# Kernel optimization log

Measured on AMD Instinct MI355X. Metric: run time of the kernel, lower is better.

## Reference

```python
import jax, jax.numpy as jnp
import numpy as np

B, S, V = 256, 512, 50000
E, PD, PS = 256, 32, 121
FN, TAG = 230, 53
FEAT = E + 2 * PD  # 320
NEG = -1e30


def setup_inputs() -> dict:
    key = jax.random.key(0)
    ks = jax.random.split(key, 12)
    sentence = jax.random.randint(ks[0], (B, S), 0, V)
    # relative-position ids; 60 marks the entity token, keep background < 60
    pos1 = jax.random.randint(ks[1], (B, S), 0, 60)
    pos2 = jax.random.randint(ks[2], (B, S), 0, 60)
    e1 = jax.random.randint(ks[3], (B,), 1, S // 3)            # entity1 in first third
    e2 = jax.random.randint(ks[4], (B,), S // 3 + 1, 2 * S // 3)  # entity2 in second third
    rows = jnp.arange(B)
    pos1 = pos1.at[rows, e1].set(60)
    pos2 = pos2.at[rows, e2].set(60)
    word_emb = 0.02 * jax.random.normal(ks[5], (V, E), dtype=jnp.float32)
    pos1_emb = 0.02 * jax.random.normal(ks[6], (PS, PD), dtype=jnp.float32)
    pos2_emb = 0.02 * jax.random.normal(ks[7], (PS, PD), dtype=jnp.float32)
    rel_emb = 0.02 * jax.random.normal(ks[8], (TAG, FN), dtype=jnp.float32)
    conv_w = 0.05 * jax.random.normal(ks[9], (3, FEAT, FN), dtype=jnp.float32)  # HIO
    conv_b = jnp.zeros((FN,), dtype=jnp.float32)
    att_weight = jax.random.normal(ks[10], (B, 1, FN), dtype=jnp.float32)
    relation_bias = jax.random.normal(ks[11], (B, TAG, 1), dtype=jnp.float32)
    return {"sentence": sentence, "pos1": pos1, "pos2": pos2,
            "word_emb": word_emb, "pos1_emb": pos1_emb, "pos2_emb": pos2_emb,
            "rel_emb": rel_emb, "conv_w": conv_w, "conv_b": conv_b,
            "att_weight": att_weight, "relation_bias": relation_bias}


def reference(sentence, pos1, pos2, word_emb, pos1_emb, pos2_emb,
              rel_emb, conv_w, conv_b, att_weight, relation_bias):
    # embedding concat: [B, S, FEAT]
    embeds = jnp.concatenate(
        [word_emb[sentence], pos1_emb[pos1], pos2_emb[pos2]], axis=2)
    # Conv2d(1, FN, (3, FEAT), padding=(1, 0)) == 1D conv over seq, SAME-ish pad 1
    cnn = jax.lax.conv_general_dilated(
        embeds, conv_w, window_strides=(1,), padding=[(1, 1)],
        dimension_numbers=("NHC", "HIO", "NHC"))  # [B, S, FN]
    cnn = jax.nn.relu(cnn + conv_b)

    # vectorized entity segment boundaries (replaces the Python batch loop)
    idx = jnp.arange(S)
    mk1 = pos1 == 60
    mk2 = pos2 == 60
    p1min = jnp.min(jnp.where(mk1, idx, S), axis=1)
    p1max = jnp.max(jnp.where(mk1, idx, -1), axis=1)
    p2min = jnp.min(jnp.where(mk2, idx, S), axis=1)
    p2max = jnp.max(jnp.where(mk2, idx, -1), axis=1)
    first = p1min < p2min
    m1 = jnp.where(first, p1min, p2min)
    m2 = jnp.where(first, p1max, p2max)
    m3 = jnp.where(first, p2min, p1min)
    m4 = jnp.where(first, p2max, p1max)

    t = idx[None, :]  # [1, S]
    mask_a = t < jnp.maximum(m1, 1)[:, None]
    mask_b = (t >= m2[:, None]) & (t < jnp.maximum(m3, m2 + 1)[:, None])
    mask_c = t >= m4[:, None]

    def seg_max(mask):
        return jnp.max(jnp.where(mask[:, :, None], cnn, NEG), axis=1)  # [B, FN]

    pcnn = jnp.stack([seg_max(mask_a), seg_max(mask_b), seg_max(mask_c)], axis=2)  # [B, FN, 3]

    # attention over the 3 pooled segments
    M = jnp.tanh(pcnn)
    scores = jnp.einsum("bof,bft->bot", att_weight, M)      # [B, 1, 3]
    a = jax.nn.softmax(scores, axis=2)
    att = jnp.einsum("bft,bot->bfo", pcnn, a)               # [B, FN, 1]
    att_out = jnp.tanh(att)

    wei = jnp.einsum("tf,bfo->bto", rel_emb, att_out)       # [B, TAG, 1]
    res = jax.nn.softmax(wei + relation_bias, axis=1)
    return res.reshape(B, -1)
```

## Files before the change

### kernel.cpp

```cpp
#include <hip/hip_runtime.h>
#include <math.h>

constexpr int B    = 256;
constexpr int S    = 512;
constexpr int E    = 256;
constexpr int PD   = 32;
constexpr int FN   = 230;
constexpr int FNP  = 256;
constexpr int TAG  = 53;
constexpr int BM   = 128;
constexpr int NG   = 10;

typedef short  bf16x8 __attribute__((ext_vector_type(8)));
typedef float  f32x4  __attribute__((ext_vector_type(4)));

__device__ __forceinline__ unsigned f2bf(float x) {
    union { float f; unsigned u; } v; v.f = x;
    unsigned r = v.u + 0x7FFF + ((v.u >> 16) & 1);
    return r >> 16;
}
__device__ __forceinline__ unsigned pack2(float a, float b) {
    return f2bf(a) | (f2bf(b) << 16);
}

__device__ __forceinline__ void gl_lds16(const void* g, void* l) {
    __builtin_amdgcn_global_load_lds(
        (const __attribute__((address_space(1))) unsigned int*)g,
        (__attribute__((address_space(3))) unsigned int*)l, 16, 0, 0);
}

constexpr size_t WS_SEGB  = 0;
constexpr size_t WS_PCNN  = 4096;
constexpr size_t WS_WT3   = 790528;
constexpr size_t WS_ZERO  = 1282048;
constexpr size_t WS_WEMB  = 1282304;
constexpr size_t WS_P1H   = 26882304;
constexpr size_t WS_P2H   = 26890048;

__global__ __launch_bounds__(256) void prep_kernel(
    const float* __restrict__ conv_w, const int* __restrict__ pos1,
    const int* __restrict__ pos2,
    const float* __restrict__ word_emb, const float* __restrict__ pos1_emb,
    const float* __restrict__ pos2_emb, char* __restrict__ ws)
{
    const int bid = blockIdx.x;
    const int tid = threadIdx.x;
    if (bid < 6250) {
        unsigned short* wembh = (unsigned short*)(ws + WS_WEMB);
        const size_t base = (size_t)bid * 2048 + tid * 8;
        float4 a = *(const float4*)(word_emb + base);
        float4 b = *(const float4*)(word_emb + base + 4);
        uint4 pk;
        pk.x = pack2(a.x, a.y); pk.y = pack2(a.z, a.w);
        pk.z = pack2(b.x, b.y); pk.w = pack2(b.z, b.w);
        *(uint4*)((unsigned short*)wembh + base) = pk;
    } else if (bid < 6254) {
        const bool isP2 = bid >= 6252;
        const int  blk  = bid - (isP2 ? 6252 : 6250);
        const float* src = isP2 ? pos2_emb : pos1_emb;
        unsigned short* dst = (unsigned short*)(ws + (isP2 ? WS_P2H : WS_P1H));
        int base = blk * 2048 + tid * 8;
        if (base + 7 < 121 * 32) {
            float4 a = *(const float4*)(src + base);
            float4 b = *(const float4*)(src + base + 4);
            uint4 pk;
            pk.x = pack2(a.x, a.y); pk.y = pack2(a.z, a.w);
            pk.z = pack2(b.x, b.y); pk.w = pack2(b.z, b.w);
            *(uint4*)(dst + base) = pk;
        }
    } else if (bid < 6494) {
        unsigned short* wt3 = (unsigned short*)(ws + WS_WT3);
        __shared__ float tile[32][33];
        const int tbid = bid - 6254;
        const int kb = tbid % 30, nb = tbid / 30;
        const int k0 = kb * 32, n0 = nb * 32;
        const int tx = tid & 31, ty = tid >> 5;
#pragma unroll
        for (int i = 0; i < 4; ++i) {
            int k = k0 + ty + i * 8, n = n0 + tx;
            tile[ty + i * 8][tx] = (n < FN) ? conv_w[(size_t)k * FN + n] : 0.0f;
        }
        __syncthreads();
        const int g = (k0 % 320) >> 5, w = k0 / 320;
        const int q = tx >> 3, e = tx & 7;
#pragma unroll
        for (int i = 0; i < 4; ++i) {
            int n = n0 + ty + i * 8;
            wt3[g * 24576 + ((w * 4 + q) * 256 + n) * 8 + e] =
                (unsigned short)f2bf(tile[tx][ty + i * 8]);
        }
    } else {
        const int b = bid - 6494;
        int* segb = (int*)(ws + WS_SEGB);
        unsigned* pcnn = (unsigned*)(ws + WS_PCNN);
        if (b == 0 && tid < 64) ((unsigned*)(ws + WS_ZERO))[tid] = 0u;
        __shared__ int r[4];
        if (tid == 0) { r[0] = S; r[1] = -1; r[2] = S; r[3] = -1; }
        __syncthreads();
        for (int s = tid; s < S; s += 256) {
            if (pos1[b * S + s] == 60) { atomicMin(&r[0], s); atomicMax(&r[1], s); }
            if (pos2[b * S + s] == 60) { atomicMin(&r[2], s); atomicMax(&r[3], s); }
        }
        __syncthreads();
        if (tid == 0) {
            int p1min = r[0], p1max = r[1], p2min = r[2], p2max = r[3];
            bool first = p1min < p2min;
            int m1 = first ? p1min : p2min;
            int m2 = first ? p1max : p2max;
            int m3 = first ? p2min : p1min;
            int m4 = first ? p2max : p1max;
            int4 o;
            o.x = max(m1, 1);
            o.y = m2;
            o.z = max(m3, m2 + 1);
            o.w = m4;
            *(int4*)(segb + b * 4) = o;
        }
        unsigned* pc = pcnn + (size_t)b * 3 * FNP;
        for (int i = tid; i < 3 * FNP; i += 256) pc[i] = 0u;
    }
}

__global__ __launch_bounds__(512, 4) void conv_mfma_kernel(
    const int* __restrict__ sentence, const int* __restrict__ pos1,
    const int* __restrict__ pos2, const float* __restrict__ conv_b,
    const char* __restrict__ ws_ro, char* __restrict__ ws)
{
    __shared__ __align__(16) unsigned short ldsB[12 * 256 * 8];
    __shared__ __align__(16) unsigned short ldsA[520 * 8];
    __shared__ unsigned maxbuf[3 * FNP];

    const unsigned short* wembh = (const unsigned short*)(ws_ro + WS_WEMB);
    const unsigned short* p1h   = (const unsigned short*)(ws_ro + WS_P1H);
    const unsigned short* p2h   = (const unsigned short*)(ws_ro + WS_P2H);
    const unsigned short* zb    = (const unsigned short*)(ws_ro + WS_ZERO);
    const char* wt3c            = ws_ro + WS_WT3;
    const int* segb             = (const int*)(ws_ro + WS_SEGB);
    unsigned* pcnn              = (unsigned*)(ws + WS_PCNN);

    const int tid  = threadIdx.x;
    const int b    = blockIdx.y;
    const int s0   = blockIdx.x * BM;
    const int lane = tid & 63;
    const int wid  = tid >> 6;
    const int wm   = wid >> 2;
    const int wn   = wid & 3;
    const int lrow = lane & 15;
    const int lgrp = lane >> 4;

    for (int i = tid; i < 3 * FNP; i += 512) maxbuf[i] = 0u;

    const int q0 = (tid >= 390) ? 3 : (tid >= 260) ? 2 : (tid >= 130) ? 1 : 0;
    const int r0 = tid - q0 * 130;
    const int sA0 = s0 - 1 + r0;
    const bool v0 = (unsigned)sA0 < (unsigned)S;
    const int sid0 = v0 ? sentence[b * S + sA0] : 0;
    const int p10  = v0 ? pos1[b * S + sA0] : 0;
    const int p20  = v0 ? pos2[b * S + sA0] : 0;
    const int r1   = 122 + tid;
    const int sA1  = s0 - 1 + r1;
    const bool v1  = (tid < 8) && ((unsigned)sA1 < (unsigned)S);
    const int sid1 = v1 ? sentence[b * S + sA1] : 0;
    const int p11  = v1 ? pos1[b * S + sA1] : 0;
    const int p21  = v1 ? pos2[b * S + sA1] : 0;

    auto srch = [&](int g, int sid, int p1v, int p2v, int qq) -> const unsigned short* {
        if (g < 8)  return wembh + (size_t)sid * E + g * 32 + qq * 8;
        if (g == 8) return p1h + p1v * PD + qq * 8;
        return p2h + p2v * PD + qq * 8;
    };

    f32x4 acc[4][4];
#pragma unroll
    for (int i = 0; i < 4; ++i)
#pragma unroll
        for (int j = 0; j < 4; ++j) acc[i][j] = (f32x4){0.f, 0.f, 0.f, 0.f};

    for (int g = 0; g < NG; ++g) {
        __builtin_amdgcn_s_barrier();
#pragma unroll
        for (int rep = 0; rep < 6; ++rep) {
            const void* src = wt3c + (size_t)g * 49152 + (size_t)(rep * 512 + tid) * 16;
            void* dst = (char*)ldsB + (rep * 512 + wid * 64) * 16;
            gl_lds16(src, dst);
        }
        {
            const unsigned short* a0 = v0 ? srch(g, sid0, p10, p20, q0) : zb;
            gl_lds16(a0, (char*)ldsA + (wid * 64) * 16);
            if (tid < 8) {
                const unsigned short* a1 = v1 ? srch(g, sid1, p11, p21, 3) : zb;
                gl_lds16(a1, (char*)ldsA + 512 * 16);
            }
        }
        asm volatile("s_waitcnt vmcnt(0)" ::: "memory");
        __builtin_amdgcn_sched_barrier(0);
        __builtin_amdgcn_s_barrier();
        __builtin_amdgcn_sched_barrier(0);
#pragma unroll
        for (int w = 0; w < 3; ++w) {
            bf16x8 af[4], bfr[4];
#pragma unroll
            for (int mi = 0; mi < 4; ++mi)
                af[mi] = *(const bf16x8*)&ldsA[(lgrp * 130 + wm * 64 + mi * 16 + lrow + w) * 8];
#pragma unroll
            for (int ni = 0; ni < 4; ++ni)
                if (wn * 64 + ni * 16 < FN)
                    bfr[ni] = *(const bf16x8*)&ldsB[((w * 4 + lgrp) * 256 + wn * 64 + ni * 16 + lrow) * 8];
            __builtin_amdgcn_s_setprio(1);
#pragma unroll
            for (int mi = 0; mi < 4; ++mi)
#pragma unroll
                for (int ni = 0; ni < 4; ++ni)
                    if (wn * 64 + ni * 16 < FN)
                        acc[mi][ni] = __builtin_amdgcn_mfma_f32_16x16x32_bf16(
                            af[mi], bfr[ni], acc[mi][ni], 0, 0, 0);
            __builtin_amdgcn_s_setprio(0);
        }
    }

    const int4 sb = *(const int4*)(segb + b * 4);
    float biasv[4];
#pragma unroll
    for (int ni = 0; ni < 4; ++ni) {
        int f = wn * 64 + ni * 16 + lrow;
        biasv[ni] = (f < FN) ? conv_b[f] : 0.0f;
    }
#pragma unroll
    for (int mi = 0; mi < 4; ++mi) {
#pragma unroll
        for (int rr = 0; rr < 4; ++rr) {
            int s = s0 + wm * 64 + mi * 16 + lgrp * 4 + rr;
            int mask = 0;
            if (s < sb.x) mask |= 1;
            if (s >= sb.y && s < sb.z) mask |= 2;
            if (s >= sb.w) mask |= 4;
            if (!mask) continue;
#pragma unroll
            for (int ni = 0; ni < 4; ++ni) {
                int f = wn * 64 + ni * 16 + lrow;
                if (f >= FN) continue;
                float v = fmaxf(acc[mi][ni][rr] + biasv[ni], 0.0f);
                unsigned uv = __float_as_uint(v);
                if (mask & 1) atomicMax(&maxbuf[f], uv);
                if (mask & 2) atomicMax(&maxbuf[FNP + f], uv);
                if (mask & 4) atomicMax(&maxbuf[2 * FNP + f], uv);
            }
        }
    }
    __syncthreads();
    unsigned* pc = pcnn + (size_t)b * 3 * FNP;
    for (int i = tid; i < 3 * FNP; i += 512) {
        unsigned m = maxbuf[i];
        if (((i & (FNP - 1)) < FN) && m) atomicMax(pc + i, m);
    }
}

__global__ __launch_bounds__(256) void finale_kernel(
    const float* __restrict__ pcnn, const float* __restrict__ att_weight,
    const float* __restrict__ rel_emb, const float* __restrict__ rel_bias,
    float* __restrict__ out)
{
    const int b = blockIdx.x;
    const int tid = threadIdx.x;
    __shared__ float red[12];
    __shared__ float satt[FN];
    __shared__ float wtag[56];

    const float* pc = pcnn + (size_t)b * 3 * FNP;
    float p0 = 0.f, p1 = 0.f, p2 = 0.f, aw = 0.f;
    if (tid < FN) {
        p0 = pc[tid];
        p1 = pc[FNP + tid];
        p2 = pc[2 * FNP + tid];
        aw = att_weight[b * FN + tid];
    }
    const int wid = tid >> 6;
#pragma unroll
    for (int t = 0; t < 3; ++t) {
        float pt = (t == 0) ? p0 : (t == 1) ? p1 : p2;
        float r = (tid < FN) ? aw * tanhf(pt) : 0.0f;
#pragma unroll
        for (int o = 32; o; o >>= 1) r += __shfl_xor(r, o);
        if ((tid & 63) == 0) red[t * 4 + wid] = r;
    }
    __syncthreads();
    float sc0 = red[0] + red[1] + red[2] + red[3];
    float sc1 = red[4] + red[5] + red[6] + red[7];
    float sc2 = red[8] + red[9] + red[10] + red[11];
    float m3s = fmaxf(sc0, fmaxf(sc1, sc2));
    float e0 = expf(sc0 - m3s), e1 = expf(sc1 - m3s), e2 = expf(sc2 - m3s);
    float inv = 1.0f / (e0 + e1 + e2);
    float a0 = e0 * inv, a1 = e1 * inv, a2 = e2 * inv;
    if (tid < FN) satt[tid] = tanhf(p0 * a0 + p1 * a1 + p2 * a2);
    __syncthreads();

    const int t = tid >> 2;
    const int part = tid & 3;
    if (t < TAG) {
        float s = 0.0f;
        for (int f = part; f < FN; f += 4) s += rel_emb[t * FN + f] * satt[f];
        s += __shfl_xor(s, 1);
        s += __shfl_xor(s, 2);
        if (part == 0) wtag[t] = s + rel_bias[b * TAG + t];
    }
    __syncthreads();

    if (tid < 64) {
        float v = (tid < TAG) ? wtag[tid] : -1e30f;
        float mx = v;
#pragma unroll
        for (int o = 32; o; o >>= 1) mx = fmaxf(mx, __shfl_xor(mx, o));
        float e = (tid < TAG) ? expf(v - mx) : 0.0f;
        float sum = e;
#pragma unroll
        for (int o = 32; o; o >>= 1) sum += __shfl_xor(sum, o);
        if (tid < TAG) out[b * TAG + tid] = e / sum;
    }
}

extern "C" void kernel_launch(void* const* d_in, const int* in_sizes, int n_in,
                              void* d_out, int out_size, void* d_ws, size_t ws_size,
                              hipStream_t stream)
{
    const int*   sentence  = (const int*)d_in[0];
    const int*   pos1      = (const int*)d_in[1];
    const int*   pos2      = (const int*)d_in[2];
    const float* word_emb  = (const float*)d_in[3];
    const float* pos1_emb  = (const float*)d_in[4];
    const float* pos2_emb  = (const float*)d_in[5];
    const float* rel_emb   = (const float*)d_in[6];
    const float* conv_w    = (const float*)d_in[7];
    const float* conv_b    = (const float*)d_in[8];
    const float* att_w     = (const float*)d_in[9];
    const float* rel_bias  = (const float*)d_in[10];
    float* out = (float*)d_out;
    char* ws = (char*)d_ws;

    prep_kernel<<<6750, 256, 0, stream>>>(
        conv_w, pos1, pos2, word_emb, pos1_emb, pos2_emb, ws);
    conv_mfma_kernel<<<dim3(S / BM, B), 512, 0, stream>>>(
        sentence, pos1, pos2, conv_b, ws, ws);
    finale_kernel<<<B, 256, 0, stream>>>(
        (const float*)(ws + WS_PCNN), att_w, rel_emb, rel_bias, out);
}
```

Before: 189.2 us.

## Double-buffer LDS staging in conv MFMA kernel and reduce segment max in registers

Adds a second LDS buffer for the weight and activation tiles, so the next group's global-to-LDS loads are issued before computing the current group, with a partial vmcnt wait. The tail-row loads are redistributed to one lane per wave. The epilogue keeps per-thread segment maxima in registers and reduces them with cross-lane shuffles before a single LDS atomicMax per feature, replacing per-element atomics. LDS use doubles and launch bounds drop to 2 blocks per CU, which lowers occupancy.

```diff
diff --git a/kernel.cpp b/kernel.cpp
--- a/kernel.cpp
+++ b/kernel.cpp
@@ -121,13 +121,13 @@
     }
 }
 
-__global__ __launch_bounds__(512, 4) void conv_mfma_kernel(
+__global__ __launch_bounds__(512, 2) void conv_mfma_kernel(
     const int* __restrict__ sentence, const int* __restrict__ pos1,
     const int* __restrict__ pos2, const float* __restrict__ conv_b,
     const char* __restrict__ ws_ro, char* __restrict__ ws)
 {
-    __shared__ __align__(16) unsigned short ldsB[12 * 256 * 8];
-    __shared__ __align__(16) unsigned short ldsA[520 * 8];
+    __shared__ __align__(16) unsigned short ldsB[2][12 * 256 * 8];
+    __shared__ __align__(16) unsigned short ldsA[2][520 * 8];
     __shared__ unsigned maxbuf[3 * FNP];
 
     const unsigned short* wembh = (const unsigned short*)(ws_ro + WS_WEMB);
@@ -157,12 +157,12 @@
     const int sid0 = v0 ? sentence[b * S + sA0] : 0;
     const int p10  = v0 ? pos1[b * S + sA0] : 0;
     const int p20  = v0 ? pos2[b * S + sA0] : 0;
-    const int r1   = 122 + tid;
-    const int sA1  = s0 - 1 + r1;
-    const bool v1  = (tid < 8) && ((unsigned)sA1 < (unsigned)S);
-    const int sid1 = v1 ? sentence[b * S + sA1] : 0;
-    const int p11  = v1 ? pos1[b * S + sA1] : 0;
-    const int p21  = v1 ? pos2[b * S + sA1] : 0;
+    const int rT   = 122 + wid;
+    const int sAT  = s0 - 1 + rT;
+    const bool vT  = (unsigned)sAT < (unsigned)S;
+    const int sidT = vT ? sentence[b * S + sAT] : 0;
+    const int p1T  = vT ? pos1[b * S + sAT] : 0;
+    const int p2T  = vT ? pos2[b * S + sAT] : 0;
 
     auto srch = [&](int g, int sid, int p1v, int p2v, int qq) -> const unsigned short* {
         if (g < 8)  return wembh + (size_t)sid * E + g * 32 + qq * 8;
@@ -170,42 +170,37 @@
         return p2h + p2v * PD + qq * 8;
     };
 
-    f32x4 acc[4][4];
-#pragma unroll
-    for (int i = 0; i < 4; ++i)
-#pragma unroll
-        for (int j = 0; j < 4; ++j) acc[i][j] = (f32x4){0.f, 0.f, 0.f, 0.f};
-
-    for (int g = 0; g < NG; ++g) {
-        __builtin_amdgcn_s_barrier();
+    auto stage = [&](int h, int g) {
 #pragma unroll
         for (int rep = 0; rep < 6; ++rep) {
             const void* src = wt3c + (size_t)g * 49152 + (size_t)(rep * 512 + tid) * 16;
-            void* dst = (char*)ldsB + (rep * 512 + wid * 64) * 16;
+            void* dst = (char*)&ldsB[h][0] + (rep * 512 + wid * 64) * 16;
             gl_lds16(src, dst);
         }
-        {
-            const unsigned short* a0 = v0 ? srch(g, sid0, p10, p20, q0) : zb;
-            gl_lds16(a0, (char*)ldsA + (wid * 64) * 16);
-            if (tid < 8) {
-                const unsigned short* a1 = v1 ? srch(g, sid1, p11, p21, 3) : zb;
-                gl_lds16(a1, (char*)ldsA + 512 * 16);
-            }
-        }
-        asm volatile("s_waitcnt vmcnt(0)" ::: "memory");
-        __builtin_amdgcn_sched_barrier(0);
-        __builtin_amdgcn_s_barrier();
-        __builtin_amdgcn_sched_barrier(0);
+        const unsigned short* a0 = v0 ? srch(g, sid0, p10, p20, q0) : zb;
+        gl_lds16(a0, (char*)&ldsA[h][0] + (wid * 64) * 16);
+        const unsigned short* aT = vT ? srch(g, sidT, p1T, p2T, 3) : zb;
+        if (lane == 0)
+            gl_lds16(aT, (char*)&ldsA[h][0] + (512 + wid) * 16);
+    };
+
+    f32x4 acc[4][4];
+#pragma unroll
+    for (int i = 0; i < 4; ++i)
+#pragma unroll
+        for (int j = 0; j < 4; ++j) acc[i][j] = (f32x4){0.f, 0.f, 0.f, 0.f};
+
+    auto compute = [&](int h) {
 #pragma unroll
         for (int w = 0; w < 3; ++w) {
             bf16x8 af[4], bfr[4];
 #pragma unroll
             for (int mi = 0; mi < 4; ++mi)
-                af[mi] = *(const bf16x8*)&ldsA[(lgrp * 130 + wm * 64 + mi * 16 + lrow + w) * 8];
+                af[mi] = *(const bf16x8*)&ldsA[h][(lgrp * 130 + wm * 64 + mi * 16 + lrow + w) * 8];
 #pragma unroll
             for (int ni = 0; ni < 4; ++ni)
                 if (wn * 64 + ni * 16 < FN)
-                    bfr[ni] = *(const bf16x8*)&ldsB[((w * 4 + lgrp) * 256 + wn * 64 + ni * 16 + lrow) * 8];
+                    bfr[ni] = *(const bf16x8*)&ldsB[h][((w * 4 + lgrp) * 256 + wn * 64 + ni * 16 + lrow) * 8];
             __builtin_amdgcn_s_setprio(1);
 #pragma unroll
             for (int mi = 0; mi < 4; ++mi)
@@ -216,7 +211,24 @@
                             af[mi], bfr[ni], acc[mi][ni], 0, 0, 0);
             __builtin_amdgcn_s_setprio(0);
         }
-    }
+    };
+
+    stage(0, 0);
+    for (int g = 0; g < NG - 1; ++g) {
+        stage((g + 1) & 1, g + 1);
+        asm volatile("s_waitcnt vmcnt(8)" ::: "memory");
+        __builtin_amdgcn_sched_barrier(0);
+        __builtin_amdgcn_s_barrier();
+        __builtin_amdgcn_sched_barrier(0);
+        compute(g & 1);
+        __builtin_amdgcn_s_barrier();
+        __builtin_amdgcn_sched_barrier(0);
+    }
+    asm volatile("s_waitcnt vmcnt(0)" ::: "memory");
+    __builtin_amdgcn_sched_barrier(0);
+    __builtin_amdgcn_s_barrier();
+    __builtin_amdgcn_sched_barrier(0);
+    compute((NG - 1) & 1);
 
     const int4 sb = *(const int4*)(segb + b * 4);
     float biasv[4];
@@ -225,26 +237,38 @@
         int f = wn * 64 + ni * 16 + lrow;
         biasv[ni] = (f < FN) ? conv_b[f] : 0.0f;
     }
+    float smax[3][4];
+#pragma unroll
+    for (int sgi = 0; sgi < 3; ++sgi)
+#pragma unroll
+        for (int ni = 0; ni < 4; ++ni) smax[sgi][ni] = 0.0f;
 #pragma unroll
     for (int mi = 0; mi < 4; ++mi) {
 #pragma unroll
         for (int rr = 0; rr < 4; ++rr) {
             int s = s0 + wm * 64 + mi * 16 + lgrp * 4 + rr;
-            int mask = 0;
-            if (s < sb.x) mask |= 1;
-            if (s >= sb.y && s < sb.z) mask |= 2;
-            if (s >= sb.w) mask |= 4;
-            if (!mask) continue;
+            bool m0 = s < sb.x;
+            bool m1 = (s >= sb.y) && (s < sb.z);
+            bool m2 = s >= sb.w;
 #pragma unroll
             for (int ni = 0; ni < 4; ++ni) {
-                int f = wn * 64 + ni * 16 + lrow;
-                if (f >= FN) continue;
                 float v = fmaxf(acc[mi][ni][rr] + biasv[ni], 0.0f);
-                unsigned uv = __float_as_uint(v);
-                if (mask & 1) atomicMax(&maxbuf[f], uv);
-                if (mask & 2) atomicMax(&maxbuf[FNP + f], uv);
-                if (mask & 4) atomicMax(&maxbuf[2 * FNP + f], uv);
+                if (m0) smax[0][ni] = fmaxf(smax[0][ni], v);
+                if (m1) smax[1][ni] = fmaxf(smax[1][ni], v);
+                if (m2) smax[2][ni] = fmaxf(smax[2][ni], v);
             }
+        }
+    }
+#pragma unroll
+    for (int sgi = 0; sgi < 3; ++sgi) {
+#pragma unroll
+        for (int ni = 0; ni < 4; ++ni) {
+            float v = smax[sgi][ni];
+            v = fmaxf(v, __shfl_xor(v, 16));
+            v = fmaxf(v, __shfl_xor(v, 32));
+            int f = wn * 64 + ni * 16 + lrow;
+            if (lgrp == 0 && f < FN)
+                atomicMax(&maxbuf[sgi * FNP + f], __float_as_uint(v));
         }
     }
     __syncthreads();
```

New measurement: 221.7 us. +17.2%, slower.
